# Kernel optimization log

Hardware: AMD Instinct MI355X
Metric: run time of the kernel (lower is better)

Reference implementation:

```python
import jax, jax.numpy as jnp
import numpy as np

N = 100000   # nodes
E = 800000   # edges
H = 256      # hidden_dim == input_dim
L = 3        # num_layers
G = 64       # graphs in batch


def setup_inputs() -> dict:
    key = jax.random.key(0)
    ks = jax.random.split(key, 16)
    s = 0.05
    inp = {
        'x': jax.random.normal(ks[0], (N, H), jnp.float32),
        'edge_index': jax.random.randint(ks[1], (2, E), 0, N, dtype=jnp.int32),
        'batch': jnp.sort(jax.random.randint(ks[2], (N,), 0, G, dtype=jnp.int32)),
        'Ws': jax.random.normal(ks[3], (L, H, H), jnp.float32) * s,
        'Wn': jax.random.normal(ks[4], (L, H, H), jnp.float32) * s,
        'bs': jnp.zeros((L, H), jnp.float32),
        'att_w': jax.random.normal(ks[5], (H, 1), jnp.float32) * s,
        'att_b': jnp.zeros((1,), jnp.float32),
        'ne_W1': jax.random.normal(ks[6], (H, H // 2), jnp.float32) * s,
        'ne_b1': jnp.zeros((H // 2,), jnp.float32),
        'ne_W2': jax.random.normal(ks[7], (H // 2, 1), jnp.float32) * s,
        'ne_b2': jnp.zeros((1,), jnp.float32),
        'nd_W1': jax.random.normal(ks[8], (H, H // 2), jnp.float32) * s,
        'nd_b1': jnp.zeros((H // 2,), jnp.float32),
        'nd_W2': jax.random.normal(ks[9], (H // 2, 1), jnp.float32) * s,
        'nd_b2': jnp.zeros((1,), jnp.float32),
    }
    return inp


def reference(x, edge_index, batch, Ws, Wn, bs, att_w, att_b,
              ne_W1, ne_b1, ne_W2, ne_b2, nd_W1, nd_b1, nd_W2, nd_b2):
    src, dst = edge_index[0], edge_index[1]
    n = x.shape[0]
    # in-degree for mean aggregation (clamped to avoid div-by-zero)
    deg = jax.ops.segment_sum(jnp.ones(src.shape[0], x.dtype), dst, num_segments=n)
    deg = jnp.maximum(deg, 1.0)[:, None]                    # [N,1]
    # GNN encoder: SAGE-mean layers, ReLU (dropout identity at eval)
    h = x
    for l in range(Ws.shape[0]):
        msg = jax.ops.segment_sum(h[src], dst, num_segments=n) / deg  # [N,H]
        h = jax.nn.relu(h @ Ws[l] + msg @ Wn[l] + bs[l])
    # attention pooling: per-graph softmax over node scores
    s = (h @ att_w + att_b)[:, 0]                           # [N]
    m = jax.ops.segment_max(s, batch, num_segments=G)
    e = jnp.exp(s - m[batch])
    denom = jax.ops.segment_sum(e, batch, num_segments=G)
    alpha = (e / denom[batch])[:, None]                     # [N,1]
    g = jax.ops.segment_sum(alpha * h, batch, num_segments=G)  # [G,H]
    # heads: Linear-ReLU-(Dropout)-Linear
    graph_logits = jax.nn.relu(g @ ne_W1 + ne_b1) @ ne_W2 + ne_b2  # [G,1]
    node_logits = jax.nn.relu(h @ nd_W1 + nd_b1) @ nd_W2 + nd_b2  # [N,1]
    return (graph_logits, node_logits)
```

## Files before the change

### kernel.cpp

```cpp
#include <hip/hip_runtime.h>
#include <hip/hip_bf16.h>

#define HID 256
#define HHALF 128

typedef unsigned short u16;
typedef __attribute__((ext_vector_type(8))) short bf16x8;
typedef __attribute__((ext_vector_type(4))) float f32x4;

__device__ __forceinline__ float bf2f(unsigned int u) {
    unsigned int x = (u & 0xffffu) << 16;
    union { unsigned int i; float f; } c; c.i = x; return c.f;
}
__device__ __forceinline__ float lof(unsigned u) {
    union { unsigned i; float f; } c; c.i = u << 16; return c.f;
}
__device__ __forceinline__ float hif(unsigned u) {
    union { unsigned i; float f; } c; c.i = u & 0xffff0000u; return c.f;
}
__device__ __forceinline__ u16 f2bf(float f) {
    __hip_bfloat16 h = __float2bfloat16(f);
    union { __hip_bfloat16 h; u16 u; } c; c.h = h; return c.u;
}

__device__ __forceinline__ void gload16(const u16* g, u16* l) {
    __builtin_amdgcn_global_load_lds(
        (const __attribute__((address_space(1))) void*)g,
        (__attribute__((address_space(3))) void*)l, 16, 0, 0);
}

__global__ void k_count(const int* __restrict__ dst, int* __restrict__ cnt, int E) {
    int i = blockIdx.x * blockDim.x + threadIdx.x;
    if (i < E) atomicAdd(&cnt[dst[i]], 1);
}

__global__ void k_scan_block(const int* __restrict__ cnt, int* __restrict__ bsum, int n) {
    __shared__ int sd[256];
    int tid = threadIdx.x;
    int i = blockIdx.x * 256 + tid;
    int v = (i < n) ? cnt[i] : 0;
    sd[tid] = v; __syncthreads();
    for (int s = 128; s > 0; s >>= 1) {
        if (tid < s) sd[tid] += sd[tid + s];
        __syncthreads();
    }
    if (tid == 0) bsum[blockIdx.x] = sd[0];
}

__global__ void k_scan_top(int* __restrict__ bsum, int nb) {
    __shared__ int sd[512];
    int t = threadIdx.x;
    int v = (t < nb) ? bsum[t] : 0;
    sd[t] = v; __syncthreads();
    for (int s = 1; s < 512; s <<= 1) {
        int x = (t >= s) ? sd[t - s] : 0;
        __syncthreads();
        sd[t] += x;
        __syncthreads();
    }
    if (t < nb) bsum[t] = sd[t] - v;
}

__global__ void k_scan_down(const int* __restrict__ cnt, const int* __restrict__ boff,
                            int* __restrict__ row_off, int n, int total) {
    __shared__ int sd[256];
    int tid = threadIdx.x;
    int i = blockIdx.x * 256 + tid;
    int v = (i < n) ? cnt[i] : 0;
    sd[tid] = v; __syncthreads();
    for (int s = 1; s < 256; s <<= 1) {
        int x = (tid >= s) ? sd[tid - s] : 0;
        __syncthreads();
        sd[tid] += x;
        __syncthreads();
    }
    if (i < n) row_off[i] = boff[blockIdx.x] + sd[tid] - v;
    if (i == 0) row_off[n] = total;
}

__global__ void k_scatter(const int* __restrict__ src, const int* __restrict__ dst,
                          const int* __restrict__ row_off, int* __restrict__ fill,
                          int* __restrict__ col, int E) {
    int i = blockIdx.x * blockDim.x + threadIdx.x;
    if (i < E) {
        int d = dst[i];
        int p = atomicAdd(&fill[d], 1);
        col[row_off[d] + p] = src[i];
    }
}

__global__ void k_f2b(const float* __restrict__ in, u16* __restrict__ o, int total4) {
    int i = blockIdx.x * blockDim.x + threadIdx.x;
    if (i >= total4) return;
    float4 v = *(const float4*)&in[(size_t)i * 4];
    uint2 p;
    p.x = (unsigned)f2bf(v.x) | ((unsigned)f2bf(v.y) << 16);
    p.y = (unsigned)f2bf(v.z) | ((unsigned)f2bf(v.w) << 16);
    *(uint2*)&o[(size_t)i * 4] = p;
}

__global__ void k_wt_all(const float* __restrict__ Ws, const float* __restrict__ Wn,
                         const float* __restrict__ ndW1,
                         u16* __restrict__ WsT, u16* __restrict__ WnT,
                         u16* __restrict__ ndW1T, int L) {
    int idx = blockIdx.x * 256 + threadIdx.x;
    int mat = idx >> 16;
    int r = idx & 65535;
    int k = r >> 8, c = r & 255;
    if (mat < L) {
        WsT[(size_t)mat * 65536 + c * 256 + k] = f2bf(Ws[(size_t)mat * 65536 + k * 256 + c]);
    } else if (mat < 2 * L) {
        int l = mat - L;
        WnT[(size_t)l * 65536 + c * 256 + k] = f2bf(Wn[(size_t)l * 65536 + k * 256 + c]);
    } else {
        if (c < HHALF) ndW1T[c * 256 + k] = f2bf(ndW1[k * HHALF + c]);
    }
}

__global__ __launch_bounds__(256) void k_agg(
    const u16* __restrict__ h, const int* __restrict__ row_off,
    const int* __restrict__ col, u16* __restrict__ msg, int n) {
    int node = blockIdx.x * 4 + (threadIdx.x >> 6);
    if (node >= n) return;
    int lane = threadIdx.x & 63;
    int half = lane >> 5;
    int t = lane & 31;
    int s0 = row_off[node], s1 = row_off[node + 1];
    float a0 = 0.f, a1 = 0.f, a2 = 0.f, a3 = 0.f;
    float a4 = 0.f, a5 = 0.f, a6 = 0.f, a7 = 0.f;
    int e = s0;
    for (; e + 4 <= s1; e += 4) {
        int c0 = col[e + half];
        int c1 = col[e + 2 + half];
        uint4 v0 = *(const uint4*)&h[(size_t)c0 * HID + t * 8];
        uint4 v1 = *(const uint4*)&h[(size_t)c1 * HID + t * 8];
        a0 += lof(v0.x) + lof(v1.x); a1 += hif(v0.x) + hif(v1.x);
        a2 += lof(v0.y) + lof(v1.y); a3 += hif(v0.y) + hif(v1.y);
        a4 += lof(v0.z) + lof(v1.z); a5 += hif(v0.z) + hif(v1.z);
        a6 += lof(v0.w) + lof(v1.w); a7 += hif(v0.w) + hif(v1.w);
    }
    for (; e < s1; e += 2) {
        if (e + half < s1) {
            int c = col[e + half];
            uint4 v = *(const uint4*)&h[(size_t)c * HID + t * 8];
            a0 += lof(v.x); a1 += hif(v.x);
            a2 += lof(v.y); a3 += hif(v.y);
            a4 += lof(v.z); a5 += hif(v.z);
            a6 += lof(v.w); a7 += hif(v.w);
        }
    }
    a0 += __shfl_xor(a0, 32); a1 += __shfl_xor(a1, 32);
    a2 += __shfl_xor(a2, 32); a3 += __shfl_xor(a3, 32);
    a4 += __shfl_xor(a4, 32); a5 += __shfl_xor(a5, 32);
    a6 += __shfl_xor(a6, 32); a7 += __shfl_xor(a7, 32);
    if (half == 0) {
        int deg = s1 - s0;
        float inv = 1.0f / (float)(deg > 1 ? deg : 1);
        uint4 o;
        o.x = (unsigned)f2bf(a0 * inv) | ((unsigned)f2bf(a1 * inv) << 16);
        o.y = (unsigned)f2bf(a2 * inv) | ((unsigned)f2bf(a3 * inv) << 16);
        o.z = (unsigned)f2bf(a4 * inv) | ((unsigned)f2bf(a5 * inv) << 16);
        o.w = (unsigned)f2bf(a6 * inv) | ((unsigned)f2bf(a7 * inv) << 16);
        *(uint4*)&msg[(size_t)node * HID + t * 8] = o;
    }
}

__global__ __launch_bounds__(512) void k_gemm_bf(
    const u16* __restrict__ A1, const u16* __restrict__ W1t,
    const u16* __restrict__ A2, const u16* __restrict__ W2t,
    const float* __restrict__ bias, u16* __restrict__ out,
    int n, int ncols) {
    __shared__ __align__(16) u16 As[128 * 32];
    __shared__ __align__(16) u16 Bs[256 * 32];
    const int tid  = threadIdx.x;
    const int lane = tid & 63;
    const int w    = tid >> 6;
    const int wr   = w >> 2, wc = w & 3;
    const int brow = blockIdx.x * 128;
    const int nkt  = A2 ? 16 : 8;

    f32x4 acc[4][4];
    #pragma unroll
    for (int m = 0; m < 4; ++m)
        #pragma unroll
        for (int q = 0; q < 4; ++q)
            acc[m][q] = (f32x4){0.f, 0.f, 0.f, 0.f};

    const int arow_t = w * 16 + (lane >> 2);
    int arow = brow + arow_t; if (arow >= n) arow = n - 1;
    const int ach = (lane & 3) ^ ((arow_t >> 1) & 3);
    const size_t abase = (size_t)arow * HID + ach * 8;
    u16* As_dst = &As[(w * 16) * 32];

    const int brow0 = w * 32 + (lane >> 2);
    const int bch0  = (lane & 3) ^ ((brow0 >> 1) & 3);
    const size_t bbase0 = (size_t)brow0 * HID + bch0 * 8;
    u16* Bs_dst0 = &Bs[(w * 32) * 32];
    const int brow1 = brow0 + 16;
    const int bch1  = (lane & 3) ^ ((brow1 >> 1) & 3);
    const size_t bbase1 = (size_t)brow1 * HID + bch1 * 8;
    u16* Bs_dst1 = &Bs[(w * 32 + 16) * 32];

    const int lr = lane & 15;
    const int lq = lane >> 4;
    const int ph = lq ^ ((lr >> 1) & 3);

    for (int kt = 0; kt < nkt; ++kt) {
        const u16* A = (kt < 8) ? A1 : A2;
        const u16* W = (kt < 8) ? W1t : W2t;
        const int k0 = (kt & 7) * 32;
        __syncthreads();
        gload16(A + abase + k0, As_dst);
        gload16(W + bbase0 + k0, Bs_dst0);
        gload16(W + bbase1 + k0, Bs_dst1);
        __syncthreads();
        bf16x8 af[4], bg[4];
        #pragma unroll
        for (int m = 0; m < 4; ++m)
            af[m] = *(const bf16x8*)&As[(wr * 64 + m * 16 + lr) * 32 + ph * 8];
        #pragma unroll
        for (int q = 0; q < 4; ++q)
            bg[q] = *(const bf16x8*)&Bs[(wc * 64 + q * 16 + lr) * 32 + ph * 8];
        #pragma unroll
        for (int m = 0; m < 4; ++m)
            #pragma unroll
            for (int q = 0; q < 4; ++q)
                acc[m][q] = __builtin_amdgcn_mfma_f32_16x16x32_bf16(
                    bg[q], af[m], acc[m][q], 0, 0, 0);
    }

    #pragma unroll
    for (int m = 0; m < 4; ++m) {
        int row = brow + wr * 64 + m * 16 + lr;
        if (row >= n) continue;
        #pragma unroll
        for (int q = 0; q < 4; ++q) {
            int col = wc * 64 + q * 16 + lq * 4;
            if (col < ncols) {
                float4 bb = *(const float4*)&bias[col];
                uint2 o;
                o.x = (unsigned)f2bf(fmaxf(acc[m][q][0] + bb.x, 0.f))
                    | ((unsigned)f2bf(fmaxf(acc[m][q][1] + bb.y, 0.f)) << 16);
                o.y = (unsigned)f2bf(fmaxf(acc[m][q][2] + bb.z, 0.f))
                    | ((unsigned)f2bf(fmaxf(acc[m][q][3] + bb.w, 0.f)) << 16);
                *(uint2*)&out[(size_t)row * ncols + col] = o;
            }
        }
    }
}

__global__ void k_score(const u16* __restrict__ h, const float* __restrict__ att_w,
                        const float* __restrict__ att_b, float* __restrict__ s, int n) {
    int gw = (blockIdx.x * blockDim.x + threadIdx.x) >> 6;
    int lane = threadIdx.x & 63;
    if (gw >= n) return;
    uint2 v = *(const uint2*)&h[(size_t)gw * HID + lane * 4];
    float4 wv = *(const float4*)&att_w[lane * 4];
    float p = bf2f(v.x) * wv.x + bf2f(v.x >> 16) * wv.y
            + bf2f(v.y) * wv.z + bf2f(v.y >> 16) * wv.w;
    #pragma unroll
    for (int off = 32; off; off >>= 1) p += __shfl_xor(p, off, 64);
    if (lane == 0) s[gw] = p + att_b[0];
}

__global__ void k_gstart(const int* __restrict__ batch, int* __restrict__ gstart, int n, int G) {
    int i = blockIdx.x * blockDim.x + threadIdx.x;
    if (i >= n) return;
    int b = batch[i];
    int bp = (i == 0) ? -1 : batch[i - 1];
    for (int g = bp + 1; g <= b; ++g) gstart[g] = i;
    if (i == n - 1) {
        for (int g = b + 1; g <= G; ++g) gstart[g] = n;
    }
}

__global__ void k_mdenom(const float* __restrict__ s, const int* __restrict__ gstart,
                         float* __restrict__ m, float* __restrict__ denom) {
    int g = blockIdx.x;
    int t = threadIdx.x;
    int i0 = gstart[g], i1 = gstart[g + 1];
    __shared__ float red[256];
    float mx = -INFINITY;
    for (int i = i0 + t; i < i1; i += 256) mx = fmaxf(mx, s[i]);
    red[t] = mx; __syncthreads();
    for (int st = 128; st; st >>= 1) {
        if (t < st) red[t] = fmaxf(red[t], red[t + st]);
        __syncthreads();
    }
    float gm = red[0];
    __syncthreads();
    float sm = 0.f;
    for (int i = i0 + t; i < i1; i += 256) sm += expf(s[i] - gm);
    red[t] = sm; __syncthreads();
    for (int st = 128; st; st >>= 1) {
        if (t < st) red[t] += red[t + st];
        __syncthreads();
    }
    if (t == 0) { m[g] = gm; denom[g] = red[0]; }
}

__global__ void k_alpha(const float* __restrict__ s, const int* __restrict__ batch,
                        const float* __restrict__ m, const float* __restrict__ denom,
                        float* __restrict__ alpha, int n) {
    int i = blockIdx.x * blockDim.x + threadIdx.x;
    if (i >= n) return;
    int b = batch[i];
    float d = denom[b];
    alpha[i] = (d > 0.f) ? expf(s[i] - m[b]) / d : 0.f;
}

__global__ void k_pool(const u16* __restrict__ h, const float* __restrict__ alpha,
                       const int* __restrict__ gstart, float* __restrict__ gpool) {
    int g = blockIdx.x, sp = blockIdx.y, t = threadIdx.x;
    int i0 = gstart[g], i1 = gstart[g + 1];
    int len = i1 - i0;
    int a = i0 + (int)((long long)len * sp / 16);
    int b = i0 + (int)((long long)len * (sp + 1) / 16);
    float acc = 0.f;
    for (int i = a; i < b; ++i) acc += alpha[i] * bf2f(h[(size_t)i * HID + t]);
    if (acc != 0.f || sp == 0) atomicAdd(&gpool[g * HID + t], acc);
}

__global__ void k_ghead(const float* __restrict__ gpool, const float* __restrict__ W1,
                        const float* __restrict__ b1, const float* __restrict__ W2,
                        const float* __restrict__ b2, float* __restrict__ out) {
    int g = blockIdx.x, t = threadIdx.x;
    __shared__ float row[HID];
    __shared__ float red[128];
    row[t] = gpool[g * HID + t];
    row[t + 128] = gpool[g * HID + t + 128];
    __syncthreads();
    float acc = 0.f;
    #pragma unroll 8
    for (int k = 0; k < HID; ++k) acc = fmaf(row[k], W1[k * HHALF + t], acc);
    float hid = fmaxf(acc + b1[t], 0.f);
    red[t] = hid * W2[t];
    __syncthreads();
    for (int st = 64; st; st >>= 1) {
        if (t < st) red[t] += red[t + st];
        __syncthreads();
    }
    if (t == 0) out[g] = red[0] + b2[0];
}

__global__ void k_ndot(const u16* __restrict__ hid, const float* __restrict__ W2,
                       const float* __restrict__ b2, float* __restrict__ out, int n) {
    int gw = (blockIdx.x * blockDim.x + threadIdx.x) >> 6;
    int lane = threadIdx.x & 63;
    if (gw >= n) return;
    unsigned v = *(const unsigned*)&hid[(size_t)gw * HHALF + lane * 2];
    float val = bf2f(v) * W2[lane * 2] + bf2f(v >> 16) * W2[lane * 2 + 1];
    #pragma unroll
    for (int off = 32; off; off >>= 1) val += __shfl_xor(val, off, 64);
    if (lane == 0) out[gw] = val + b2[0];
}

extern "C" void kernel_launch(void* const* d_in, const int* in_sizes, int n_in,
                              void* d_out, int out_size, void* d_ws, size_t ws_size,
                              hipStream_t stream) {
    const float* x      = (const float*)d_in[0];
    const int*   eidx   = (const int*)d_in[1];
    const int*   batch  = (const int*)d_in[2];
    const float* Ws     = (const float*)d_in[3];
    const float* Wn     = (const float*)d_in[4];
    const float* bs     = (const float*)d_in[5];
    const float* att_w  = (const float*)d_in[6];
    const float* att_b  = (const float*)d_in[7];
    const float* ne_W1  = (const float*)d_in[8];
    const float* ne_b1  = (const float*)d_in[9];
    const float* ne_W2  = (const float*)d_in[10];
    const float* ne_b2  = (const float*)d_in[11];
    const float* nd_W1  = (const float*)d_in[12];
    const float* nd_b1  = (const float*)d_in[13];
    const float* nd_W2  = (const float*)d_in[14];
    const float* nd_b2  = (const float*)d_in[15];
    float* out = (float*)d_out;

    const int N = in_sizes[2];
    const int E = in_sizes[1] / 2;
    const int L = in_sizes[3] / (HID * HID);
    const int G = out_size - N;

    const int* src = eidx;
    const int* dst = eidx + E;

    size_t off = 0;
    auto alloc = [&](size_t bytes) {
        void* p = (char*)d_ws + off;
        off += (bytes + 255) & ~(size_t)255;
        return p;
    };
    int*   cnt     = (int*)alloc((size_t)N * 4);
    int*   row_off = (int*)alloc((size_t)(N + 1) * 4);
    int*   fill    = (int*)alloc((size_t)N * 4);
    int*   col     = (int*)alloc((size_t)E * 4);
    int*   gstart  = (int*)alloc((size_t)(G + 1) * 4);
    int*   bsum    = (int*)alloc(1024 * 4);
    float* sarr    = (float*)alloc((size_t)N * 4);
    float* alpha   = (float*)alloc((size_t)N * 4);
    float* marr    = (float*)alloc((size_t)G * 4);
    float* denom   = (float*)alloc((size_t)G * 4);
    float* gpool   = (float*)alloc((size_t)G * HID * 4);
    u16*   xb      = (u16*)alloc((size_t)N * HID * 2);
    u16*   msgb    = (u16*)alloc((size_t)N * HID * 2);
    u16*   hb1     = (u16*)alloc((size_t)N * HID * 2);
    u16*   hb2     = (u16*)alloc((size_t)N * HID * 2);
    u16*   hidb    = (u16*)alloc((size_t)N * HHALF * 2);
    u16*   WsT     = (u16*)alloc((size_t)L * HID * HID * 2);
    u16*   WnT     = (u16*)alloc((size_t)L * HID * HID * 2);
    u16*   ndW1T   = (u16*)alloc((size_t)HID * HID * 2);
    (void)ws_size;

    const int eb = (E + 255) / 256;
    const int nb = (N + 255) / 256;

    hipMemsetAsync(cnt, 0, (size_t)N * 4, stream);
    k_count<<<eb, 256, 0, stream>>>(dst, cnt, E);
    k_scan_block<<<nb, 256, 0, stream>>>(cnt, bsum, N);
    k_scan_top<<<1, 512, 0, stream>>>(bsum, nb);
    k_scan_down<<<nb, 256, 0, stream>>>(cnt, bsum, row_off, N, E);
    hipMemsetAsync(fill, 0, (size_t)N * 4, stream);
    k_scatter<<<eb, 256, 0, stream>>>(src, dst, row_off, fill, col, E);

    k_f2b<<<(N * HID / 4 + 255) / 256, 256, 0, stream>>>(x, xb, N * HID / 4);
    k_wt_all<<<(2 * L + 1) * (HID * HID / 256), 256, 0, stream>>>(
        Ws, Wn, nd_W1, WsT, WnT, ndW1T, L);

    const int gx = (N + 127) / 128;
    const u16* hin = xb;
    u16* hout = hb1;
    for (int l = 0; l < L; ++l) {
        k_agg<<<(N + 3) / 4, 256, 0, stream>>>(hin, row_off, col, msgb, N);
        k_gemm_bf<<<gx, 512, 0, stream>>>(
            hin, WsT + (size_t)l * HID * HID, msgb, WnT + (size_t)l * HID * HID,
            bs + (size_t)l * HID, hout, N, HID);
        hin = hout;
        hout = (hout == hb1) ? hb2 : hb1;
    }
    const u16* h = hin;

    k_score<<<(N + 3) / 4, 256, 0, stream>>>(h, att_w, att_b, sarr, N);
    k_gstart<<<nb, 256, 0, stream>>>(batch, gstart, N, G);
    k_mdenom<<<G, 256, 0, stream>>>(sarr, gstart, marr, denom);
    k_alpha<<<nb, 256, 0, stream>>>(sarr, batch, marr, denom, alpha, N);
    hipMemsetAsync(gpool, 0, (size_t)G * HID * 4, stream);
    k_pool<<<dim3(G, 16), HID, 0, stream>>>(h, alpha, gstart, gpool);

    k_ghead<<<G, HHALF, 0, stream>>>(gpool, ne_W1, ne_b1, ne_W2, ne_b2, out);

    k_gemm_bf<<<gx, 512, 0, stream>>>(
        h, ndW1T, nullptr, nullptr, nd_b1, hidb, N, HHALF);
    k_ndot<<<(N + 3) / 4, 256, 0, stream>>>(hidb, nd_W2, nd_b2, out + G, N);
}
```

Before: 586.4 us.

## Double-buffer GEMM LDS tiles with async prefetch and unroll aggregation loop

The GEMM kernel now keeps two LDS buffers and issues global-to-LDS loads two k-tiles ahead. It uses explicit vmcnt waits and scheduling-pinned barriers so memory latency overlaps with MFMA work. The aggregation kernel also processes eight edges per iteration instead of four, giving more loads in flight. The cost is double the shared memory per block, which may reduce occupancy, and the correctness of the hand-written vmcnt counts depends on the exact instruction ordering.

```diff
diff --git a/kernel.cpp b/kernel.cpp
--- a/kernel.cpp
+++ b/kernel.cpp
@@ -27,6 +27,11 @@
     __builtin_amdgcn_global_load_lds(
         (const __attribute__((address_space(1))) void*)g,
         (__attribute__((address_space(3))) void*)l, 16, 0, 0);
+}
+__device__ __forceinline__ void pinned_barrier() {
+    __builtin_amdgcn_sched_barrier(0);
+    __builtin_amdgcn_s_barrier();
+    __builtin_amdgcn_sched_barrier(0);
 }
 
 __global__ void k_count(const int* __restrict__ dst, int* __restrict__ cnt, int E) {
@@ -129,15 +134,23 @@
     float a0 = 0.f, a1 = 0.f, a2 = 0.f, a3 = 0.f;
     float a4 = 0.f, a5 = 0.f, a6 = 0.f, a7 = 0.f;
     int e = s0;
-    for (; e + 4 <= s1; e += 4) {
+    for (; e + 8 <= s1; e += 8) {
         int c0 = col[e + half];
         int c1 = col[e + 2 + half];
+        int c2 = col[e + 4 + half];
+        int c3 = col[e + 6 + half];
         uint4 v0 = *(const uint4*)&h[(size_t)c0 * HID + t * 8];
         uint4 v1 = *(const uint4*)&h[(size_t)c1 * HID + t * 8];
-        a0 += lof(v0.x) + lof(v1.x); a1 += hif(v0.x) + hif(v1.x);
-        a2 += lof(v0.y) + lof(v1.y); a3 += hif(v0.y) + hif(v1.y);
-        a4 += lof(v0.z) + lof(v1.z); a5 += hif(v0.z) + hif(v1.z);
-        a6 += lof(v0.w) + lof(v1.w); a7 += hif(v0.w) + hif(v1.w);
+        uint4 v2 = *(const uint4*)&h[(size_t)c2 * HID + t * 8];
+        uint4 v3 = *(const uint4*)&h[(size_t)c3 * HID + t * 8];
+        a0 += (lof(v0.x) + lof(v1.x)) + (lof(v2.x) + lof(v3.x));
+        a1 += (hif(v0.x) + hif(v1.x)) + (hif(v2.x) + hif(v3.x));
+        a2 += (lof(v0.y) + lof(v1.y)) + (lof(v2.y) + lof(v3.y));
+        a3 += (hif(v0.y) + hif(v1.y)) + (hif(v2.y) + hif(v3.y));
+        a4 += (lof(v0.z) + lof(v1.z)) + (lof(v2.z) + lof(v3.z));
+        a5 += (hif(v0.z) + hif(v1.z)) + (hif(v2.z) + hif(v3.z));
+        a6 += (lof(v0.w) + lof(v1.w)) + (lof(v2.w) + lof(v3.w));
+        a7 += (hif(v0.w) + hif(v1.w)) + (hif(v2.w) + hif(v3.w));
     }
     for (; e < s1; e += 2) {
         if (e + half < s1) {
@@ -170,8 +183,8 @@
     const u16* __restrict__ A2, const u16* __restrict__ W2t,
     const float* __restrict__ bias, u16* __restrict__ out,
     int n, int ncols) {
-    __shared__ __align__(16) u16 As[128 * 32];
-    __shared__ __align__(16) u16 Bs[256 * 32];
+    __shared__ __align__(16) u16 As[2][128 * 32];
+    __shared__ __align__(16) u16 Bs[2][256 * 32];
     const int tid  = threadIdx.x;
     const int lane = tid & 63;
     const int w    = tid >> 6;
@@ -190,43 +203,57 @@
     int arow = brow + arow_t; if (arow >= n) arow = n - 1;
     const int ach = (lane & 3) ^ ((arow_t >> 1) & 3);
     const size_t abase = (size_t)arow * HID + ach * 8;
-    u16* As_dst = &As[(w * 16) * 32];
+    const int As_off = (w * 16) * 32;
 
     const int brow0 = w * 32 + (lane >> 2);
     const int bch0  = (lane & 3) ^ ((brow0 >> 1) & 3);
     const size_t bbase0 = (size_t)brow0 * HID + bch0 * 8;
-    u16* Bs_dst0 = &Bs[(w * 32) * 32];
+    const int Bs_off0 = (w * 32) * 32;
     const int brow1 = brow0 + 16;
     const int bch1  = (lane & 3) ^ ((brow1 >> 1) & 3);
     const size_t bbase1 = (size_t)brow1 * HID + bch1 * 8;
-    u16* Bs_dst1 = &Bs[(w * 32 + 16) * 32];
+    const int Bs_off1 = (w * 32 + 16) * 32;
 
     const int lr = lane & 15;
     const int lq = lane >> 4;
     const int ph = lq ^ ((lr >> 1) & 3);
 
+    auto stage = [&](int t) {
+        const u16* A = (t < 8) ? A1 : A2;
+        const u16* W = (t < 8) ? W1t : W2t;
+        const int k0 = (t & 7) * 32;
+        const int b = t & 1;
+        gload16(A + abase + k0, &As[b][As_off]);
+        gload16(W + bbase0 + k0, &Bs[b][Bs_off0]);
+        gload16(W + bbase1 + k0, &Bs[b][Bs_off1]);
+    };
+
+    stage(0);
+    stage(1);
+
     for (int kt = 0; kt < nkt; ++kt) {
-        const u16* A = (kt < 8) ? A1 : A2;
-        const u16* W = (kt < 8) ? W1t : W2t;
-        const int k0 = (kt & 7) * 32;
-        __syncthreads();
-        gload16(A + abase + k0, As_dst);
-        gload16(W + bbase0 + k0, Bs_dst0);
-        gload16(W + bbase1 + k0, Bs_dst1);
-        __syncthreads();
+        if (kt == nkt - 1) {
+            asm volatile("s_waitcnt vmcnt(0)" ::: "memory");
+        } else {
+            asm volatile("s_waitcnt vmcnt(3)" ::: "memory");
+        }
+        pinned_barrier();
+        const int b = kt & 1;
         bf16x8 af[4], bg[4];
         #pragma unroll
         for (int m = 0; m < 4; ++m)
-            af[m] = *(const bf16x8*)&As[(wr * 64 + m * 16 + lr) * 32 + ph * 8];
+            af[m] = *(const bf16x8*)&As[b][(wr * 64 + m * 16 + lr) * 32 + ph * 8];
         #pragma unroll
         for (int q = 0; q < 4; ++q)
-            bg[q] = *(const bf16x8*)&Bs[(wc * 64 + q * 16 + lr) * 32 + ph * 8];
+            bg[q] = *(const bf16x8*)&Bs[b][(wc * 64 + q * 16 + lr) * 32 + ph * 8];
         #pragma unroll
         for (int m = 0; m < 4; ++m)
             #pragma unroll
             for (int q = 0; q < 4; ++q)
                 acc[m][q] = __builtin_amdgcn_mfma_f32_16x16x32_bf16(
                     bg[q], af[m], acc[m][q], 0, 0, 0);
+        pinned_barrier();
+        if (kt + 2 < nkt) stage(kt + 2);
     }
 
     #pragma unroll
```

Result: slower. 657.0 us (+12.0%).
